# Kernel tuning notes

Measured on AMD Instinct MI355X. Metric: run time of the kernel, lower is better.

## Reference

```python
import jax, jax.numpy as jnp
import numpy as np

D_MODEL = 2048
N_HEADS = 16
HEAD_DIM = D_MODEL // N_HEADS
B, T = 2, 2048


def setup_inputs() -> dict:
    key = jax.random.key(0)
    ks = jax.random.split(key, 5)
    s = 1.0 / np.sqrt(D_MODEL)
    x = jax.random.normal(ks[0], (B, T, D_MODEL), dtype=jnp.float32)
    Wq = jax.random.uniform(ks[1], (D_MODEL, D_MODEL), jnp.float32, -s, s)
    Wk = jax.random.uniform(ks[2], (D_MODEL, D_MODEL), jnp.float32, -s, s)
    Wv = jax.random.uniform(ks[3], (D_MODEL, D_MODEL), jnp.float32, -s, s)
    Wo = jax.random.uniform(ks[4], (D_MODEL, D_MODEL), jnp.float32, -s, s)
    return {"x": x, "Wq": Wq, "Wk": Wk, "Wv": Wv, "Wo": Wo}


def _alibi_bias(n_heads: int, seq_len: int) -> jnp.ndarray:
    # slopes_h = 0.5 ** (h * 8 / n_heads), h = 1..n_heads
    exponents = jnp.arange(1, n_heads + 1, dtype=jnp.float32)
    slopes = 0.5 ** (exponents * 8.0 / n_heads)  # (H,)
    pos = jnp.arange(seq_len, dtype=jnp.float32)
    rel = pos[None, :] - pos[:, None]  # (T,T), rel[i,j] = j - i
    bias = slopes[:, None, None] * rel[None]  # (H,T,T)
    causal = pos[None, :] <= pos[:, None]  # j <= i
    return jnp.where(causal[None], bias, -jnp.inf)


def reference(x, Wq, Wk, Wv, Wo):
    Bsz, Tlen, _ = x.shape
    H, D = N_HEADS, HEAD_DIM
    # projections (nn.Linear: x @ W.T); split heads -> (B,H,T,D)
    def split_heads(t):
        return t.reshape(Bsz, Tlen, H, D).transpose(0, 2, 1, 3)
    q = split_heads(x @ Wq.T)
    k = split_heads(x @ Wk.T)
    v = split_heads(x @ Wv.T)
    scale = jnp.sqrt(jnp.float32(D))
    scores = jnp.einsum('bhqd,bhkd->bhqk', q, k) / scale  # (B,H,T,T)
    scores = scores + _alibi_bias(H, Tlen)[None]
    attn = jax.nn.softmax(scores, axis=-1)
    out = jnp.einsum('bhqk,bhkd->bhqd', attn, v)
    out = out.transpose(0, 2, 1, 3).reshape(Bsz, Tlen, H * D)
    return out @ Wo.T
```

## Files before the change

kernel.cpp:

```cpp
#include <hip/hip_runtime.h>
#include <stdint.h>

#define D_MODEL 2048
#define N_HEADS 16
#define HEAD_D  128
#define BATCH   2
#define SEQ     2048
#define MTOT    (BATCH*SEQ)

typedef __bf16 bf16x8 __attribute__((ext_vector_type(8)));
typedef float  f32x4  __attribute__((ext_vector_type(4)));
typedef unsigned short u16x8 __attribute__((ext_vector_type(8)));
typedef unsigned short u16x4 __attribute__((ext_vector_type(4)));

#define MFMA16(a,b,c) __builtin_amdgcn_mfma_f32_16x16x32_bf16(a, b, c, 0, 0, 0)

__device__ __forceinline__ unsigned short f2bf(float f) {
  unsigned u = __builtin_bit_cast(unsigned, f);
  u += 0x7fffu + ((u >> 16) & 1u);
  return (unsigned short)(u >> 16);
}

__device__ __forceinline__ bf16x8 ld_frag(const unsigned short* p) {
  u16x8 raw = *(const u16x8*)p;
  return __builtin_bit_cast(bf16x8, raw);
}

__device__ __forceinline__ void gload16(const void* g, void* lds) {
  __builtin_amdgcn_global_load_lds(
      (const __attribute__((address_space(1))) unsigned int*)g,
      (__attribute__((address_space(3))) unsigned int*)lds, 16, 0, 0);
}

__global__ __launch_bounds__(256) void f32_to_bf16_k(const float* __restrict__ in,
                                                     unsigned short* __restrict__ out,
                                                     int n8) {
  int i = blockIdx.x * 256 + threadIdx.x;
  if (i >= n8) return;
  const float4* p = (const float4*)in + (size_t)i * 2;
  float4 a = p[0], b = p[1];
  u16x8 o;
  o[0] = f2bf(a.x); o[1] = f2bf(a.y); o[2] = f2bf(a.z); o[3] = f2bf(a.w);
  o[4] = f2bf(b.x); o[5] = f2bf(b.y); o[6] = f2bf(b.z); o[7] = f2bf(b.w);
  *((u16x8*)out + i) = o;
}

__global__ __launch_bounds__(256) void f32_to_bf16_w4(const float* __restrict__ w0,
                                                      const float* __restrict__ w1,
                                                      const float* __restrict__ w2,
                                                      const float* __restrict__ w3,
                                                      unsigned short* __restrict__ out) {
  const int i = blockIdx.x * 256 + threadIdx.x;
  const int which = i >> 19;
  const int r = i & ((1 << 19) - 1);
  const float* s = (which == 0) ? w0 : (which == 1) ? w1 : (which == 2) ? w2 : w3;
  const float4* p = (const float4*)s + (size_t)r * 2;
  float4 a = p[0], b = p[1];
  u16x8 o;
  o[0] = f2bf(a.x); o[1] = f2bf(a.y); o[2] = f2bf(a.z); o[3] = f2bf(a.w);
  o[4] = f2bf(b.x); o[5] = f2bf(b.y); o[6] = f2bf(b.z); o[7] = f2bf(b.w);
  *((u16x8*)out + i) = o;
}

__global__ __launch_bounds__(256) void gemm_bt_f32(const unsigned short* __restrict__ A,
                                                   const unsigned short* __restrict__ B,
                                                   float* __restrict__ C,
                                                   int M, int N, int K) {
  __shared__ __align__(16) unsigned short As[128 * 32];
  __shared__ __align__(16) unsigned short Bs[128 * 32];
  const int tid  = threadIdx.x;
  const int lane = tid & 63;
  const int w    = tid >> 6;
  const int wr   = w >> 1, wc = w & 1;

  const int gx = gridDim.x;
  int bx = blockIdx.x, by = blockIdx.y;
  const int nwg = gx * gridDim.y;
  if ((nwg & 7) == 0) {
    const int lid = by * gx + bx;
    const int cpx = nwg >> 3;
    const int swz = (lid & 7) * cpx + (lid >> 3);
    bx = swz % gx; by = swz / gx;
  }
  const int brow = by * 128;
  const int bcol = bx * 128;

  const int e0 = (w * 2) * 512 + lane * 8;
  const int e1 = (w * 2 + 1) * 512 + lane * 8;
  const int r0 = e0 >> 5, cc0 = e0 & 31;
  const int r1 = e1 >> 5, cc1 = e1 & 31;
  const unsigned short* Ap0 = A + (size_t)(brow + r0) * K + cc0;
  const unsigned short* Ap1 = A + (size_t)(brow + r1) * K + cc1;
  const unsigned short* Bp0 = B + (size_t)(bcol + r0) * K + cc0;
  const unsigned short* Bp1 = B + (size_t)(bcol + r1) * K + cc1;
  unsigned short* As0 = &As[(w * 2) * 512];
  unsigned short* As1 = &As[(w * 2 + 1) * 512];
  unsigned short* Bs0 = &Bs[(w * 2) * 512];
  unsigned short* Bs1 = &Bs[(w * 2 + 1) * 512];

  f32x4 acc[4][4] = {};
  const int la = lane & 15;
  const int lb = (lane >> 4) * 8;

  for (int kt = 0; kt < K; kt += 32) {
    gload16(Ap0 + kt, As0);
    gload16(Ap1 + kt, As1);
    gload16(Bp0 + kt, Bs0);
    gload16(Bp1 + kt, Bs1);
    __syncthreads();
    bf16x8 af[4], bfr[4];
#pragma unroll
    for (int m = 0; m < 4; ++m)
      af[m] = ld_frag(&As[(wr * 64 + m * 16 + la) * 32 + lb]);
#pragma unroll
    for (int n = 0; n < 4; ++n)
      bfr[n] = ld_frag(&Bs[(wc * 64 + n * 16 + la) * 32 + lb]);
#pragma unroll
    for (int m = 0; m < 4; ++m)
#pragma unroll
      for (int n = 0; n < 4; ++n)
        acc[m][n] = MFMA16(af[m], bfr[n], acc[m][n]);
    __syncthreads();
  }

  const int rowb = (lane >> 4) * 4;
#pragma unroll
  for (int m = 0; m < 4; ++m)
#pragma unroll
    for (int n = 0; n < 4; ++n) {
      const int gcol = bcol + wc * 64 + n * 16 + la;
      const int grow0 = brow + wr * 64 + m * 16 + rowb;
#pragma unroll
      for (int j = 0; j < 4; ++j)
        C[(size_t)(grow0 + j) * N + gcol] = acc[m][n][j];
    }
}

#define SQ_STAGE_HALF(T2, HF)                                                     \
  do {                                                                            \
    const int kt2_ = (T2) * 64;                                                   \
    _Pragma("unroll")                                                             \
    for (int s_ = 0; s_ < 2; ++s_) {                                              \
      const int idx_ = s_ * 512 + tid;                                            \
      const int sub_ = idx_ >> 6;                                                 \
      const int rin_ = (idx_ >> 2) & 15;                                          \
      const int cby_ = (idx_ & 3) * 16;                                           \
      const int r_   = ((HF) & 1) * 128 + (sub_ >> 1) * 16 + rin_;                \
      const int ce_  = (sub_ & 1) * 32 + ((cby_ ^ ((rin_ & 8) << 2)) >> 1);       \
      const unsigned short* gp_ = ((HF) < 2)                                      \
          ? (Ag + (size_t)(brow + r_) * 2048 + kt2_ + ce_)                        \
          : (Bg + (size_t)(bcol + r_) * 2048 + kt2_ + ce_);                       \
      gload16(gp_, SB + ((((T2) & 1) * 65536 + ((HF) >> 1) * 32768 +              \
                          ((HF) & 1) * 16384 + (s_ * 512 + w * 64) * 16) >> 1));  \
    }                                                                             \
  } while (0)

#define SQ_STAGE_ALL(T2)                                                          \
  do { SQ_STAGE_HALF(T2, 0); SQ_STAGE_HALF(T2, 1);                                \
       SQ_STAGE_HALF(T2, 2); SQ_STAGE_HALF(T2, 3); } while (0)

#define SQ_MFMA16x(AF, BF, MOFF)                                                  \
  do {                                                                            \
    __builtin_amdgcn_s_setprio(1);                                                \
    _Pragma("unroll") for (int m_ = 0; m_ < 4; ++m_)                              \
      _Pragma("unroll") for (int n_ = 0; n_ < 4; ++n_)                            \
        acc[(MOFF) + m_][n_] = MFMA16(AF[m_], BF[n_], acc[(MOFF) + m_][n_]);      \
    __builtin_amdgcn_s_setprio(0);                                                \
  } while (0)

#define SQ_TILE(CUR)                                                              \
  do {                                                                            \
    const char* Ab_ = (const char*)SB + (CUR) * 65536 + wr * 16384;               \
    const char* Bb_ = (const char*)SB + (CUR) * 65536 + 32768 +                   \
                      (wcn >> 1) * 16384 + (wcn & 1) * 8192;                      \
    bf16x8 a0_[4], a1_[4], a2_[4], a3_[4], b0_[4], b1_[4];                        \
    _Pragma("unroll") for (int n_ = 0; n_ < 4; ++n_)                              \
      b0_[n_] = ld_frag((const unsigned short*)(Bb_ + n_ * 2048 + la * 64 + cxa));\
    _Pragma("unroll") for (int m_ = 0; m_ < 4; ++m_)                              \
      a0_[m_] = ld_frag((const unsigned short*)(Ab_ + m_ * 2048 + la * 64 + cxa));\
    _Pragma("unroll") for (int m_ = 0; m_ < 4; ++m_)                              \
      a1_[m_] = ld_frag((const unsigned short*)(Ab_ + (4 + m_) * 2048 + la * 64 + cxa)); \
    asm volatile("s_waitcnt lgkmcnt(4)" ::: "memory");                            \
    __builtin_amdgcn_sched_barrier(0);                                            \
    SQ_MFMA16x(a0_, b0_, 0);                                                      \
    _Pragma("unroll") for (int n_ = 0; n_ < 4; ++n_)                              \
      b1_[n_] = ld_frag((const unsigned short*)(Bb_ + n_ * 2048 + 1024 + la * 64 + cxa)); \
    _Pragma("unroll") for (int m_ = 0; m_ < 4; ++m_)                              \
      a2_[m_] = ld_frag((const unsigned short*)(Ab_ + m_ * 2048 + 1024 + la * 64 + cxa)); \
    asm volatile("s_waitcnt lgkmcnt(8)" ::: "memory");                            \
    __builtin_amdgcn_sched_barrier(0);                                            \
    SQ_MFMA16x(a1_, b0_, 4);                                                      \
    _Pragma("unroll") for (int m_ = 0; m_ < 4; ++m_)                              \
      a3_[m_] = ld_frag((const unsigned short*)(Ab_ + (4 + m_) * 2048 + 1024 + la * 64 + cxa)); \
    asm volatile("s_waitcnt lgkmcnt(4)" ::: "memory");                            \
    __builtin_amdgcn_sched_barrier(0);                                            \
    SQ_MFMA16x(a2_, b1_, 0);                                                      \
    asm volatile("s_waitcnt lgkmcnt(0)" ::: "memory");                            \
    __builtin_amdgcn_sched_barrier(0);                                            \
    SQ_MFMA16x(a3_, b1_, 4);                                                      \
  } while (0)

__global__ __launch_bounds__(512, 1)
__attribute__((amdgpu_waves_per_eu(1, 2)))
void gemm_qkv256(const unsigned short* __restrict__ Ag,
                 const unsigned short* __restrict__ Bg,
                 unsigned short* __restrict__ Qp,
                 unsigned short* __restrict__ Kp,
                 unsigned short* __restrict__ Vtp) {
  __shared__ __align__(16) unsigned short SB[65536];
  const int tid = threadIdx.x, lane = tid & 63, w = tid >> 6;
  const int wr = w >> 2, wcn = w & 3;
  const int la = lane & 15, hi = lane >> 4;
  const int cxa = (hi * 16) ^ ((lane & 8) << 2);

  const int gx = gridDim.x;
  const int nwg = gx * gridDim.y;
  const int lid = blockIdx.y * gx + blockIdx.x;
  const int cpx = nwg >> 3;
  const int sz = (lid & 7) * cpx + (lid >> 3);
  const int bx = sz % gx, by = sz / gx;
  const int brow = by * 256, bcol = bx * 256;

  f32x4 acc[8][4] = {};

  SQ_STAGE_ALL(0);

#pragma unroll 1
  for (int t = 0; t < 32; ++t) {
    const int cur = t & 1;
    if (t < 31) {
      SQ_STAGE_ALL(t + 1);
      asm volatile("s_waitcnt vmcnt(8)" ::: "memory");
    } else {
      asm volatile("s_waitcnt vmcnt(0)" ::: "memory");
    }
    __builtin_amdgcn_sched_barrier(0);
    __builtin_amdgcn_s_barrier();

    SQ_TILE(cur);

    __builtin_amdgcn_s_barrier();
  }

#pragma unroll
  for (int mg = 0; mg < 8; ++mg) {
#pragma unroll
    for (int ng = 0; ng < 4; ++ng) {
      const int gcol = bcol + wcn * 64 + ng * 16 + la;
      const int grow0 = brow + wr * 128 + mg * 16 + hi * 4;
      const int which = gcol >> 11;
      const int c2 = gcol & 2047;
      const int hh = c2 >> 7, dd = c2 & 127;
      const int bb = grow0 >> 11, tt = grow0 & (SEQ - 1);
      if (which == 2) {
        u16x4 pk;
#pragma unroll
        for (int j = 0; j < 4; ++j) pk[j] = f2bf(acc[mg][ng][j]);
        *(u16x4*)&Vtp[(((size_t)bb * N_HEADS + hh) * HEAD_D + dd) * SEQ + tt] = pk;
      } else {
        unsigned short* dst = which ? Kp : Qp;
#pragma unroll
        for (int j = 0; j < 4; ++j)
          dst[(((size_t)bb * N_HEADS + hh) * SEQ + tt + j) * HEAD_D + dd] = f2bf(acc[mg][ng][j]);
      }
    }
  }
}


#define STAGE_KV1(U)                                                                \
  do {                                                                              \
    const int kv0_ = (((U) <= qtA) ? (U) : (U) - qtA - 1) * 64;                     \
    _Pragma("unroll")                                                               \
    for (int s = 0; s < 4; ++s) {                                                   \
      const int p_ = (w * 4 + s) * 1024 + lane * 16;                                \
      const int row_ = p_ >> 8, cb_ = p_ & 255;                                     \
      const int col_ = (cb_ ^ ((row_ & 7) << 4)) >> 1;                              \
      gload16(&K[kbase + (size_t)(kv0_ + row_) * HEAD_D + col_],                    \
              &Ks[(w * 4 + s) * 512]);                                              \
    }                                                                               \
    _Pragma("unroll")                                                               \
    for (int s = 0; s < 4; ++s) {                                                   \
      const int p_ = (w * 4 + s) * 1024 + lane * 16;                                \
      const int d_ = p_ >> 7, cb_ = p_ & 127;                                       \
      const int col_ = (cb_ ^ ((d_ & 7) << 4)) >> 1;                                \
      gload16(&VT[vtbase + (size_t)d_ * SEQ + kv0_ + col_],                         \
              &Vs[(w * 4 + s) * 512]);                                              \
    }                                                                               \
  } while (0)

#define LOAD_Q(Q0)                                                                  \
  do {                                                                              \
    const size_t qa_ = ((size_t)bh * SEQ + (Q0) + w * 16 + la) * HEAD_D + lq * 8;   \
    _Pragma("unroll")                                                               \
    for (int kk = 0; kk < 4; ++kk) qf[kk] = ld_frag(&Q[qa_ + kk * 32]);             \
  } while (0)

#define EPILOGUE(Q0)                                                                \
  do {                                                                              \
    _Pragma("unroll")                                                               \
    for (int j = 0; j < 4; ++j) {                                                   \
      const float inv_ = 1.0f / lrow[j];                                            \
      const int q_ = (Q0) + w * 16 + lq * 4 + j;                                    \
      const size_t ob_ = ((size_t)b * SEQ + q_) * D_MODEL + (size_t)h * HEAD_D;     \
      _Pragma("unroll")                                                             \
      for (int n = 0; n < 8; ++n) O[ob_ + n * 16 + la] = f2bf(acc[n][j] * inv_);    \
    }                                                                               \
  } while (0)

#define SOFTMAX_TILE(S, QG0, DIAG, KV0)                                            \
  do {                                                                             \
    float corr_[4];                                                                \
    float pe_[4][4];                                                               \
    _Pragma("unroll")                                                              \
    for (int j = 0; j < 4; ++j) {                                                  \
      const int qgj_ = (QG0) + j;                                                  \
      float mx_ = -1e30f;                                                          \
      _Pragma("unroll")                                                            \
      for (int c = 0; c < 4; ++c) {                                                \
        const int kvg_ = (KV0) + c * 16 + la;                                      \
        float sv_ = fmaf(S[c][j], scale, slope * (float)(kvg_ - qgj_));            \
        if ((DIAG) && (kvg_ > qgj_)) sv_ = -1e30f;                                 \
        pe_[c][j] = sv_;                                                           \
        mx_ = fmaxf(mx_, sv_);                                                     \
      }                                                                            \
      mx_ = fmaxf(mx_, __shfl_xor(mx_, 1));                                        \
      mx_ = fmaxf(mx_, __shfl_xor(mx_, 2));                                        \
      mx_ = fmaxf(mx_, __shfl_xor(mx_, 4));                                        \
      mx_ = fmaxf(mx_, __shfl_xor(mx_, 8));                                        \
      const float nm_ = fmaxf(mrow[j], mx_);                                       \
      const float cr_ = __expf(mrow[j] - nm_);                                     \
      corr_[j] = cr_;                                                              \
      float rs_ = 0.f;                                                             \
      _Pragma("unroll")                                                            \
      for (int c = 0; c < 4; ++c) {                                                \
        const float e_ = __expf(pe_[c][j] - nm_);                                  \
        pe_[c][j] = e_;                                                            \
        rs_ += e_;                                                                 \
      }                                                                            \
      rs_ += __shfl_xor(rs_, 1);                                                   \
      rs_ += __shfl_xor(rs_, 2);                                                   \
      rs_ += __shfl_xor(rs_, 4);                                                   \
      rs_ += __shfl_xor(rs_, 8);                                                   \
      lrow[j] = lrow[j] * cr_ + rs_;                                               \
      mrow[j] = nm_;                                                               \
    }                                                                              \
    _Pragma("unroll")                                                              \
    for (int n = 0; n < 8; ++n) {                                                  \
      _Pragma("unroll")                                                            \
      for (int j = 0; j < 4; ++j) acc[n][j] *= corr_[j];                           \
    }                                                                              \
    _Pragma("unroll")                                                              \
    for (int c = 0; c < 4; ++c) {                                                  \
      _Pragma("unroll")                                                            \
      for (int j = 0; j < 4; ++j) {                                                \
        const int row_ = lq * 4 + j;                                               \
        const int cb_ = (c * 16 + la) * 2;                                         \
        *(unsigned short*)((char*)Ps[w] + row_ * 128 + (cb_ ^ ((row_ & 7) << 4)))  \
            = f2bf(pe_[c][j]);                                                     \
      }                                                                            \
    }                                                                              \
  } while (0)

__global__ __launch_bounds__(256)
void attn_k(const unsigned short* __restrict__ Q,
            const unsigned short* __restrict__ K,
            const unsigned short* __restrict__ VT,
            unsigned short* __restrict__ O) {
  __shared__ __align__(16) unsigned short Ks[64 * HEAD_D];
  __shared__ __align__(16) unsigned short Vs[HEAD_D * 64];
  __shared__ __align__(16) unsigned short Ps[4][16 * 64];

  const int tid = threadIdx.x, lane = tid & 63, w = tid >> 6;
  const int lid = blockIdx.x;
  const int swz = (lid & 7) * 64 + (lid >> 3);
  const int qp = swz & 15;
  const int h  = (swz >> 4) & 15;
  const int b  = swz >> 8;
  const int bh = b * N_HEADS + h;
  const int qtA = qp, qtB = 31 - qp;
  const int q0A = qtA * 64, q0B = qtB * 64;

  const float slope = exp2f(-0.5f * (float)(h + 1));
  const float scale = 0.08838834764831845f;
  const int la = lane & 15;
  const int lq = lane >> 4;

  const size_t kbase  = (size_t)bh * SEQ * HEAD_D;
  const size_t vtbase = (size_t)bh * HEAD_D * SEQ;

  bf16x8 qf[4];
  f32x4 acc[8] = {};
  float mrow[4] = {-1e30f, -1e30f, -1e30f, -1e30f};
  float lrow[4] = {0.f, 0.f, 0.f, 0.f};
  int q0cur = q0A;

  LOAD_Q(q0A);
  STAGE_KV1(0);

  for (int u = 0; u < 33; ++u) {
    asm volatile("s_waitcnt vmcnt(0)" ::: "memory");
    __builtin_amdgcn_sched_barrier(0);
    __builtin_amdgcn_s_barrier();

    if (u == qtA + 1) {
      EPILOGUE(q0A);
      LOAD_Q(q0B);
      q0cur = q0B;
#pragma unroll
      for (int n = 0; n < 8; ++n)
#pragma unroll
        for (int j = 0; j < 4; ++j) acc[n][j] = 0.f;
#pragma unroll
      for (int j = 0; j < 4; ++j) { mrow[j] = -1e30f; lrow[j] = 0.f; }
    }

    const int kv0 = ((u <= qtA) ? u : u - qtA - 1) * 64;
    const bool diag = (u == qtA) || (u == 32);

    f32x4 s4[4] = {{0.f,0.f,0.f,0.f},{0.f,0.f,0.f,0.f},{0.f,0.f,0.f,0.f},{0.f,0.f,0.f,0.f}};
    __builtin_amdgcn_s_setprio(1);
#pragma unroll
    for (int c = 0; c < 4; ++c) {
      const int row = c * 16 + la;
#pragma unroll
      for (int kk = 0; kk < 4; ++kk) {
        const int cb = kk * 64 + lq * 16;
        bf16x8 kf = ld_frag((const unsigned short*)((const char*)Ks + row * 256 + (cb ^ ((row & 7) << 4))));
        s4[c] = MFMA16(qf[kk], kf, s4[c]);
      }
    }
    __builtin_amdgcn_s_setprio(0);

    SOFTMAX_TILE(s4, q0cur + w * 16 + lq * 4, diag, kv0);

    asm volatile("s_waitcnt lgkmcnt(0)" ::: "memory");
    __builtin_amdgcn_sched_barrier(0);

    __builtin_amdgcn_s_setprio(1);
#pragma unroll
    for (int kk = 0; kk < 2; ++kk) {
      const int pcb = kk * 64 + lq * 16;
      const int paddr = la * 128 + (pcb ^ ((la & 7) << 4));
      bf16x8 pf = ld_frag((const unsigned short*)((const char*)Ps[w] + paddr));
#pragma unroll
      for (int n = 0; n < 8; ++n) {
        const int d = n * 16 + la;
        bf16x8 vf = ld_frag((const unsigned short*)((const char*)Vs + d * 128 + (pcb ^ ((d & 7) << 4))));
        acc[n] = MFMA16(pf, vf, acc[n]);
      }
    }
    __builtin_amdgcn_s_setprio(0);

    __builtin_amdgcn_s_barrier();
    if (u < 32) STAGE_KV1(u + 1);
  }

  EPILOGUE(q0B);
}

extern "C" void kernel_launch(void* const* d_in, const int* in_sizes, int n_in,
                              void* d_out, int out_size, void* d_ws, size_t ws_size,
                              hipStream_t stream) {
  (void)in_sizes; (void)n_in; (void)out_size; (void)ws_size;
  const float* x  = (const float*)d_in[0];
  const float* Wq = (const float*)d_in[1];
  const float* Wk = (const float*)d_in[2];
  const float* Wv = (const float*)d_in[3];
  const float* Wo = (const float*)d_in[4];

  char* ws = (char*)d_ws;
  unsigned short* xb = (unsigned short*)(ws + 0);
  unsigned short* wq = (unsigned short*)(ws + 16777216);
  unsigned short* wo = (unsigned short*)(ws + 41943040);
  unsigned short* q  = (unsigned short*)(ws + 50331648);
  unsigned short* k  = (unsigned short*)(ws + 67108864);
  unsigned short* vt = (unsigned short*)(ws + 83886080);
  unsigned short* o  = (unsigned short*)(ws + 0);

  f32_to_bf16_k<<<4096, 256, 0, stream>>>(x, xb, (MTOT * D_MODEL) / 8);
  f32_to_bf16_w4<<<8192, 256, 0, stream>>>(Wq, Wk, Wv, Wo, wq);

  gemm_qkv256<<<dim3(3 * D_MODEL / 256, MTOT / 256), 512, 0, stream>>>(xb, wq, q, k, vt);

  attn_k<<<512, 256, 0, stream>>>(q, k, vt, o);

  dim3 g2(D_MODEL / 128, MTOT / 128);
  gemm_bt_f32<<<g2, 256, 0, stream>>>(o, wo, (float*)d_out, MTOT, D_MODEL, D_MODEL);
}
```

Before: 295.3 us.

## Double attention KV tile to 128 and fuse bf16 conversion launches

The attention kernel now stages 128 keys and values per loop step instead of 64. That halves the iteration count, along with the barriers and vmcnt waits per query pair, and the softmax and PV loops are widened to match. Separately, the x and weight fp32-to-bf16 conversions are merged into a single launch that writes the contiguous workspace region. The cost is more LDS (about 80KB per block) and more registers, which may lower occupancy. Less of the staging latency may be hidden inside each step.

```diff
diff --git a/kernel.cpp b/kernel.cpp
--- a/kernel.cpp
+++ b/kernel.cpp
@@ -32,28 +32,23 @@
       (__attribute__((address_space(3))) unsigned int*)lds, 16, 0, 0);
 }
 
-__global__ __launch_bounds__(256) void f32_to_bf16_k(const float* __restrict__ in,
-                                                     unsigned short* __restrict__ out,
-                                                     int n8) {
-  int i = blockIdx.x * 256 + threadIdx.x;
-  if (i >= n8) return;
-  const float4* p = (const float4*)in + (size_t)i * 2;
-  float4 a = p[0], b = p[1];
-  u16x8 o;
-  o[0] = f2bf(a.x); o[1] = f2bf(a.y); o[2] = f2bf(a.z); o[3] = f2bf(a.w);
-  o[4] = f2bf(b.x); o[5] = f2bf(b.y); o[6] = f2bf(b.z); o[7] = f2bf(b.w);
-  *((u16x8*)out + i) = o;
-}
-
-__global__ __launch_bounds__(256) void f32_to_bf16_w4(const float* __restrict__ w0,
-                                                      const float* __restrict__ w1,
-                                                      const float* __restrict__ w2,
-                                                      const float* __restrict__ w3,
-                                                      unsigned short* __restrict__ out) {
+__global__ __launch_bounds__(256) void f32_to_bf16_all(const float* __restrict__ x,
+                                                       const float* __restrict__ w0,
+                                                       const float* __restrict__ w1,
+                                                       const float* __restrict__ w2,
+                                                       const float* __restrict__ w3,
+                                                       unsigned short* __restrict__ out) {
   const int i = blockIdx.x * 256 + threadIdx.x;
-  const int which = i >> 19;
-  const int r = i & ((1 << 19) - 1);
-  const float* s = (which == 0) ? w0 : (which == 1) ? w1 : (which == 2) ? w2 : w3;
+  const float* s;
+  int r;
+  if (i < (1 << 20)) {
+    s = x; r = i;
+  } else {
+    const int j = i - (1 << 20);
+    const int which = j >> 19;
+    r = j & ((1 << 19) - 1);
+    s = (which == 0) ? w0 : (which == 1) ? w1 : (which == 2) ? w2 : w3;
+  }
   const float4* p = (const float4*)s + (size_t)r * 2;
   float4 a = p[0], b = p[1];
   u16x8 o;
@@ -268,24 +263,24 @@
 }
 
 
-#define STAGE_KV1(U)                                                                \
+#define STAGE_KV128(U)                                                              \
   do {                                                                              \
-    const int kv0_ = (((U) <= qtA) ? (U) : (U) - qtA - 1) * 64;                     \
+    const int kv0_ = (((U) < nA) ? (U) : (U) - nA) * 128;                           \
     _Pragma("unroll")                                                               \
-    for (int s = 0; s < 4; ++s) {                                                   \
-      const int p_ = (w * 4 + s) * 1024 + lane * 16;                                \
+    for (int s = 0; s < 8; ++s) {                                                   \
+      const int p_ = (w * 8 + s) * 1024 + lane * 16;                                \
       const int row_ = p_ >> 8, cb_ = p_ & 255;                                     \
       const int col_ = (cb_ ^ ((row_ & 7) << 4)) >> 1;                              \
       gload16(&K[kbase + (size_t)(kv0_ + row_) * HEAD_D + col_],                    \
-              &Ks[(w * 4 + s) * 512]);                                              \
+              &Ks[(w * 8 + s) * 512]);                                              \
     }                                                                               \
     _Pragma("unroll")                                                               \
-    for (int s = 0; s < 4; ++s) {                                                   \
-      const int p_ = (w * 4 + s) * 1024 + lane * 16;                                \
-      const int d_ = p_ >> 7, cb_ = p_ & 127;                                       \
-      const int col_ = (cb_ ^ ((d_ & 7) << 4)) >> 1;                                \
-      gload16(&VT[vtbase + (size_t)d_ * SEQ + kv0_ + col_],                         \
-              &Vs[(w * 4 + s) * 512]);                                              \
+    for (int s = 0; s < 8; ++s) {                                                   \
+      const int p_ = (w * 8 + s) * 1024 + lane * 16;                                \
+      const int row_ = p_ >> 8, cb_ = p_ & 255;                                     \
+      const int col_ = (cb_ ^ ((row_ & 7) << 4)) >> 1;                              \
+      gload16(&VT[vtbase + (size_t)row_ * SEQ + kv0_ + col_],                       \
+              &Vs[(w * 8 + s) * 512]);                                              \
     }                                                                               \
   } while (0)
 
@@ -308,16 +303,16 @@
     }                                                                               \
   } while (0)
 
-#define SOFTMAX_TILE(S, QG0, DIAG, KV0)                                            \
+#define SOFTMAX_TILE128(S, QG0, DIAG, KV0)                                         \
   do {                                                                             \
     float corr_[4];                                                                \
-    float pe_[4][4];                                                               \
+    float pe_[8][4];                                                               \
     _Pragma("unroll")                                                              \
     for (int j = 0; j < 4; ++j) {                                                  \
       const int qgj_ = (QG0) + j;                                                  \
       float mx_ = -1e30f;                                                          \
       _Pragma("unroll")                                                            \
-      for (int c = 0; c < 4; ++c) {                                                \
+      for (int c = 0; c < 8; ++c) {                                                \
         const int kvg_ = (KV0) + c * 16 + la;                                      \
         float sv_ = fmaf(S[c][j], scale, slope * (float)(kvg_ - qgj_));            \
         if ((DIAG) && (kvg_ > qgj_)) sv_ = -1e30f;                                 \
@@ -333,7 +328,7 @@
       corr_[j] = cr_;                                                              \
       float rs_ = 0.f;                                                             \
       _Pragma("unroll")                                                            \
-      for (int c = 0; c < 4; ++c) {                                                \
+      for (int c = 0; c < 8; ++c) {                                                \
         const float e_ = __expf(pe_[c][j] - nm_);                                  \
         pe_[c][j] = e_;                                                            \
         rs_ += e_;                                                                 \
@@ -351,12 +346,12 @@
       for (int j = 0; j < 4; ++j) acc[n][j] *= corr_[j];                           \
     }                                                                              \
     _Pragma("unroll")                                                              \
-    for (int c = 0; c < 4; ++c) {                                                  \
+    for (int c = 0; c < 8; ++c) {                                                  \
       _Pragma("unroll")                                                            \
       for (int j = 0; j < 4; ++j) {                                                \
         const int row_ = lq * 4 + j;                                               \
         const int cb_ = (c * 16 + la) * 2;                                         \
-        *(unsigned short*)((char*)Ps[w] + row_ * 128 + (cb_ ^ ((row_ & 7) << 4)))  \
+        *(unsigned short*)((char*)Ps[w] + row_ * 256 + (cb_ ^ ((row_ & 7) << 4)))  \
             = f2bf(pe_[c][j]);                                                     \
       }                                                                            \
     }                                                                              \
@@ -367,9 +362,9 @@
             const unsigned short* __restrict__ K,
             const unsigned short* __restrict__ VT,
             unsigned short* __restrict__ O) {
-  __shared__ __align__(16) unsigned short Ks[64 * HEAD_D];
-  __shared__ __align__(16) unsigned short Vs[HEAD_D * 64];
-  __shared__ __align__(16) unsigned short Ps[4][16 * 64];
+  __shared__ __align__(16) unsigned short Ks[128 * 128];
+  __shared__ __align__(16) unsigned short Vs[128 * 128];
+  __shared__ __align__(16) unsigned short Ps[4][16 * 128];
 
   const int tid = threadIdx.x, lane = tid & 63, w = tid >> 6;
   const int lid = blockIdx.x;
@@ -380,6 +375,7 @@
   const int bh = b * N_HEADS + h;
   const int qtA = qp, qtB = 31 - qp;
   const int q0A = qtA * 64, q0B = qtB * 64;
+  const int nA = (qp >> 1) + 1;
 
   const float slope = exp2f(-0.5f * (float)(h + 1));
   const float scale = 0.08838834764831845f;
@@ -396,14 +392,14 @@
   int q0cur = q0A;
 
   LOAD_Q(q0A);
-  STAGE_KV1(0);
-
-  for (int u = 0; u < 33; ++u) {
+  STAGE_KV128(0);
+
+  for (int u = 0; u < 17; ++u) {
     asm volatile("s_waitcnt vmcnt(0)" ::: "memory");
     __builtin_amdgcn_sched_barrier(0);
     __builtin_amdgcn_s_barrier();
 
-    if (u == qtA + 1) {
+    if (u == nA) {
       EPILOGUE(q0A);
       LOAD_Q(q0B);
       q0cur = q0B;
@@ -415,13 +411,13 @@
       for (int j = 0; j < 4; ++j) { mrow[j] = -1e30f; lrow[j] = 0.f; }
     }
 
-    const int kv0 = ((u <= qtA) ? u : u - qtA - 1) * 64;
-    const bool diag = (u == qtA) || (u == 32);
-
-    f32x4 s4[4] = {{0.f,0.f,0.f,0.f},{0.f,0.f,0.f,0.f},{0.f,0.f,0.f,0.f},{0.f,0.f,0.f,0.f}};
+    const int kv0 = ((u < nA) ? u : u - nA) * 128;
+    const bool diag = (u == nA - 1) || (u == 16);
+
+    f32x4 s4[8] = {};
     __builtin_amdgcn_s_setprio(1);
 #pragma unroll
-    for (int c = 0; c < 4; ++c) {
+    for (int c = 0; c < 8; ++c) {
       const int row = c * 16 + la;
 #pragma unroll
       for (int kk = 0; kk < 4; ++kk) {
@@ -432,28 +428,28 @@
     }
     __builtin_amdgcn_s_setprio(0);
 
-    SOFTMAX_TILE(s4, q0cur + w * 16 + lq * 4, diag, kv0);
+    SOFTMAX_TILE128(s4, q0cur + w * 16 + lq * 4, diag, kv0);
 
     asm volatile("s_waitcnt lgkmcnt(0)" ::: "memory");
     __builtin_amdgcn_sched_barrier(0);
 
     __builtin_amdgcn_s_setprio(1);
 #pragma unroll
-    for (int kk = 0; kk < 2; ++kk) {
+    for (int kk = 0; kk < 4; ++kk) {
       const int pcb = kk * 64 + lq * 16;
-      const int paddr = la * 128 + (pcb ^ ((la & 7) << 4));
+      const int paddr = la * 256 + (pcb ^ ((la & 7) << 4));
       bf16x8 pf = ld_frag((const unsigned short*)((const char*)Ps[w] + paddr));
 #pragma unroll
       for (int n = 0; n < 8; ++n) {
         const int d = n * 16 + la;
-        bf16x8 vf = ld_frag((const unsigned short*)((const char*)Vs + d * 128 + (pcb ^ ((d & 7) << 4))));
+        bf16x8 vf = ld_frag((const unsigned short*)((const char*)Vs + d * 256 + (pcb ^ ((d & 7) << 4))));
         acc[n] = MFMA16(pf, vf, acc[n]);
       }
     }
     __builtin_amdgcn_s_setprio(0);
 
     __builtin_amdgcn_s_barrier();
-    if (u < 32) STAGE_KV1(u + 1);
+    if (u < 16) STAGE_KV128(u + 1);
   }
 
   EPILOGUE(q0B);
@@ -478,8 +474,7 @@
   unsigned short* vt = (unsigned short*)(ws + 83886080);
   unsigned short* o  = (unsigned short*)(ws + 0);
 
-  f32_to_bf16_k<<<4096, 256, 0, stream>>>(x, xb, (MTOT * D_MODEL) / 8);
-  f32_to_bf16_w4<<<8192, 256, 0, stream>>>(Wq, Wk, Wv, Wo, wq);
+  f32_to_bf16_all<<<12288, 256, 0, stream>>>(x, Wq, Wk, Wv, Wo, xb);
 
   gemm_qkv256<<<dim3(3 * D_MODEL / 256, MTOT / 256), 512, 0, stream>>>(xb, wq, q, k, vt);
 
```

Result: slower. 328.9 us (+11.4%).
